# Kernel optimization log

Measured on AMD Instinct MI355X. Metric: run time of the kernel, lower is better.

## Reference

```python
import jax, jax.numpy as jnp
import numpy as np

D_MODEL = 1024
N_HEADS = 16
HEAD_DIM = D_MODEL // N_HEADS


def setup_inputs() -> dict:
    key = jax.random.key(0)
    ks = jax.random.split(key, 5)
    B, T = 4, 4096
    x = jax.random.normal(ks[0], (B, T, D_MODEL), dtype=jnp.float32)
    s = 1.0 / np.sqrt(D_MODEL)
    Wqkv = jax.random.normal(ks[1], (D_MODEL, 3 * D_MODEL), dtype=jnp.float32) * s
    bqkv = jnp.zeros((3 * D_MODEL,), dtype=jnp.float32)
    Wout = jax.random.normal(ks[2], (D_MODEL, D_MODEL), dtype=jnp.float32) * s
    bout = jnp.zeros((D_MODEL,), dtype=jnp.float32)
    return {"x": x, "Wqkv": Wqkv, "bqkv": bqkv, "Wout": Wout, "bout": bout}


def _feature_map(x):
    # elu(x) + 1  (strictly positive feature map)
    return jax.nn.elu(x) + 1.0


def reference(x, Wqkv, bqkv, Wout, bout):
    B, T, C = x.shape
    H, D = N_HEADS, HEAD_DIM
    qkv = x @ Wqkv + bqkv                      # [B,T,3C]
    qkv = qkv.reshape(B, T, 3, H, D)
    qkv = jnp.transpose(qkv, (2, 0, 3, 1, 4))  # [3,B,H,T,D]
    q, k, v = qkv[0], qkv[1], qkv[2]
    scale = D ** 0.25
    q_m = _feature_map(q / scale)
    k_m = _feature_map(k / scale)
    kv = jnp.einsum('bhtd,bhtm->bhdm', k_m, v)     # [B,H,D,D]
    out = jnp.einsum('bhtd,bhdm->bhtm', q_m, kv)   # [B,H,T,D]
    z = q_m.sum(axis=-1, keepdims=True)            # note: sum over feature dim (as in source)
    out = out / (z + 1e-6)
    out = jnp.transpose(out, (0, 2, 1, 3)).reshape(B, T, C)
    return out @ Wout + bout
```

## Files before the change

### kernel.cpp

```cpp
#include <hip/hip_runtime.h>
#include <hip/hip_bf16.h>
#include <math.h>

#define B_ 4
#define T_ 4096
#define H_ 16
#define D_ 64
#define C_ 1024
#define BT_ (B_*T_)

using short8  = __attribute__((ext_vector_type(8))) short;
using floatx4 = __attribute__((ext_vector_type(4))) float;

__device__ __forceinline__ float feature_map(float x) {
    return x > 0.0f ? x + 1.0f : __expf(x);
}
__device__ __forceinline__ unsigned short f2bf(float x) {
    union { __hip_bfloat16 b; unsigned short u; } c;
    c.b = __float2bfloat16(x);
    return c.u;
}
__device__ __forceinline__ float bf2f(unsigned short u) {
    union { unsigned int u; float f; } c;
    c.u = (unsigned)u << 16;
    return c.f;
}
__device__ __forceinline__ void async16(const void* g, void* l) {
    __builtin_amdgcn_global_load_lds(
        (const __attribute__((address_space(1))) void*)g,
        (__attribute__((address_space(3))) void*)l, 16, 0, 0);
}

__global__ __launch_bounds__(256)
void convert_x_kernel(const float4* __restrict__ x, ushort* __restrict__ xb)
{
    const size_t i = (size_t)blockIdx.x * 256 + threadIdx.x;
    const float4 v = x[i];
    *reinterpret_cast<ushort4*>(&xb[i * 4]) =
        make_ushort4(f2bf(v.x), f2bf(v.y), f2bf(v.z), f2bf(v.w));
}

__global__ __launch_bounds__(256)
void transpose_bf16_kernel(const float* __restrict__ W, ushort* __restrict__ WT,
                           int K, int N)
{
    __shared__ float t[32][33];
    const int n0 = blockIdx.x * 32, k0 = blockIdx.y * 32;
    const int r = threadIdx.x >> 5, c = threadIdx.x & 31;
    #pragma unroll
    for (int i = 0; i < 4; i++)
        t[r + 8 * i][c] = W[(size_t)(k0 + r + 8 * i) * N + n0 + c];
    __syncthreads();
    #pragma unroll
    for (int i = 0; i < 4; i++)
        WT[(size_t)(n0 + r + 8 * i) * K + k0 + c] = f2bf(t[c][r + 8 * i]);
}

__global__ __launch_bounds__(256)
void kv_mfma_kernel(const ushort* __restrict__ xb, const ushort* __restrict__ WqkvT,
                    const float* __restrict__ bqkv, float* __restrict__ kv)
{
    __shared__ __align__(16) unsigned char smem[34816];
    ushort* As = (ushort*)smem;
    ushort* Bs = (ushort*)(smem + 8192);
    ushort* kT = (ushort*)smem;
    ushort* vT = kT + 64 * 136;

    const int tid = threadIdx.x;
    const int w = tid >> 6, l = tid & 63;
    const int wm = w >> 1, wn = w & 1;
    const int lr = l & 15, quad = l >> 4;
    const int lk8 = quad * 8;
    const int h = blockIdx.x;
    const int mBase = blockIdx.y * 128;
    const int bb = mBase >> 12;

    const int srow = w * 32 + (l >> 2);
    const int scol = (l & 3) * 8;
    const ushort* gA = xb + (size_t)(mBase + srow) * C_ + scol;
    const int br0 = (srow < 64)      ? (C_ + h * 64 + srow)      : (2 * C_ + h * 64 + srow - 64);
    const int br1 = (srow + 16 < 64) ? (C_ + h * 64 + srow + 16) : (2 * C_ + h * 64 + srow - 48);
    const ushort* gB0 = WqkvT + (size_t)br0 * C_ + scol;
    const ushort* gB1 = WqkvT + (size_t)br1 * C_ + scol;
    void* ldsA = (void*)(smem + w * 2048);
    void* ldsB = (void*)(smem + 8192 + w * 2048);

    floatx4 acc[4][4];
    #pragma unroll
    for (int i = 0; i < 4; i++)
        #pragma unroll
        for (int j = 0; j < 4; j++) acc[i][j] = (floatx4)0.0f;

    for (int k0 = 0; k0 < C_; k0 += 32) {
        __syncthreads();
        async16(gA + k0, ldsA);
        async16(gA + 16 * C_ + k0, (void*)((char*)ldsA + 1024));
        async16(gB0 + k0, ldsB);
        async16(gB1 + k0, (void*)((char*)ldsB + 1024));
        __syncthreads();

        short8 af[4], bf[4];
        #pragma unroll
        for (int mt = 0; mt < 4; mt++)
            af[mt] = *(const short8*)&As[(wm * 64 + mt * 16 + lr) * 32 + lk8];
        #pragma unroll
        for (int nt = 0; nt < 4; nt++)
            bf[nt] = *(const short8*)&Bs[(wn * 64 + nt * 16 + lr) * 32 + lk8];
        #pragma unroll
        for (int mt = 0; mt < 4; mt++)
            #pragma unroll
            for (int nt = 0; nt < 4; nt++)
                acc[mt][nt] = __builtin_amdgcn_mfma_f32_16x16x32_bf16(
                    af[mt], bf[nt], acc[mt][nt], 0, 0, 0);
    }

    const float inv_scale = 0.35355339059327373f;
    const int bbias = (wn ? 2 * C_ : C_) + h * 64;

    __syncthreads();
    {
        ushort* dst = wn ? vT : kT;
        #pragma unroll
        for (int nt = 0; nt < 4; nt++) {
            const int cc = nt * 16 + lr;
            const float bv = bqkv[bbias + cc];
            #pragma unroll
            for (int mt = 0; mt < 4; mt++) {
                float v0 = acc[mt][nt][0] + bv, v1 = acc[mt][nt][1] + bv;
                float v2 = acc[mt][nt][2] + bv, v3 = acc[mt][nt][3] + bv;
                if (wn == 0) {
                    v0 = feature_map(v0 * inv_scale); v1 = feature_map(v1 * inv_scale);
                    v2 = feature_map(v2 * inv_scale); v3 = feature_map(v3 * inv_scale);
                }
                *(ushort4*)&dst[cc * 136 + wm * 64 + mt * 16 + quad * 4] =
                    make_ushort4(f2bf(v0), f2bf(v1), f2bf(v2), f2bf(v3));
            }
        }
    }
    __syncthreads();

    floatx4 acc2[2][2];
    #pragma unroll
    for (int i = 0; i < 2; i++)
        #pragma unroll
        for (int j = 0; j < 2; j++) acc2[i][j] = (floatx4)0.0f;

    #pragma unroll
    for (int kst = 0; kst < 4; kst++) {
        short8 afr[2], bfr[2];
        #pragma unroll
        for (int i = 0; i < 2; i++)
            afr[i] = *(const short8*)&kT[(wm * 32 + i * 16 + lr) * 136 + kst * 32 + lk8];
        #pragma unroll
        for (int j = 0; j < 2; j++)
            bfr[j] = *(const short8*)&vT[(wn * 32 + j * 16 + lr) * 136 + kst * 32 + lk8];
        #pragma unroll
        for (int i = 0; i < 2; i++)
            #pragma unroll
            for (int j = 0; j < 2; j++)
                acc2[i][j] = __builtin_amdgcn_mfma_f32_16x16x32_bf16(
                    afr[i], bfr[j], acc2[i][j], 0, 0, 0);
    }

    float* kvb = kv + (size_t)(bb * H_ + h) * (D_ * D_);
    #pragma unroll
    for (int i = 0; i < 2; i++)
        #pragma unroll
        for (int j = 0; j < 2; j++)
            #pragma unroll
            for (int r = 0; r < 4; r++) {
                const int d = wm * 32 + i * 16 + quad * 4 + r;
                const int m = wn * 32 + j * 16 + lr;
                atomicAdd(&kvb[d * 64 + m], acc2[i][j][r]);
            }
}

__global__ __launch_bounds__(256)
void qattn_mfma_kernel(const ushort* __restrict__ xb, const ushort* __restrict__ WqkvT,
                       const float* __restrict__ bqkv, const float* __restrict__ kv,
                       ushort* __restrict__ attn)
{
    __shared__ __align__(16) unsigned char smem[54272];
    ushort* As  = (ushort*)smem;
    ushort* Bs  = (ushort*)(smem + 8192);
    ushort* qS  = (ushort*)smem;
    ushort* kvT = (ushort*)(smem + 34816);
    float*  zS  = (float*)(smem + 53248);

    const int tid = threadIdx.x;
    const int w = tid >> 6, l = tid & 63;
    const int wm = w >> 1, wn = w & 1;
    const int lr = l & 15, quad = l >> 4;
    const int lk8 = quad * 8;
    const int hp = blockIdx.x;
    const int mBase = blockIdx.y * 128;
    const int bb = mBase >> 12;

    {
        const float* kvg = kv + ((size_t)bb * H_ + hp * 2) * (D_ * D_);
        #pragma unroll
        for (int e = 0; e < 32; e++) {
            const int flat = e * 256 + tid;
            const int hh = flat >> 12, d = (flat >> 6) & 63, m = flat & 63;
            kvT[hh * 4608 + m * 72 + d] = f2bf(kvg[flat]);
        }
    }

    const int srow = w * 32 + (l >> 2);
    const int scol = (l & 3) * 8;
    const ushort* gA = xb + (size_t)(mBase + srow) * C_ + scol;
    const ushort* gB = WqkvT + (size_t)(hp * 128 + srow) * C_ + scol;
    void* ldsA = (void*)(smem + w * 2048);
    void* ldsB = (void*)(smem + 8192 + w * 2048);

    floatx4 acc[4][4];
    #pragma unroll
    for (int i = 0; i < 4; i++)
        #pragma unroll
        for (int j = 0; j < 4; j++) acc[i][j] = (floatx4)0.0f;

    for (int k0 = 0; k0 < C_; k0 += 32) {
        __syncthreads();
        async16(gA + k0, ldsA);
        async16(gA + 16 * C_ + k0, (void*)((char*)ldsA + 1024));
        async16(gB + k0, ldsB);
        async16(gB + 16 * C_ + k0, (void*)((char*)ldsB + 1024));
        __syncthreads();

        short8 af[4], bfr[4];
        #pragma unroll
        for (int mt = 0; mt < 4; mt++)
            af[mt] = *(const short8*)&As[(wm * 64 + mt * 16 + lr) * 32 + lk8];
        #pragma unroll
        for (int nt = 0; nt < 4; nt++)
            bfr[nt] = *(const short8*)&Bs[(wn * 64 + nt * 16 + lr) * 32 + lk8];
        #pragma unroll
        for (int mt = 0; mt < 4; mt++)
            #pragma unroll
            for (int nt = 0; nt < 4; nt++)
                acc[mt][nt] = __builtin_amdgcn_mfma_f32_16x16x32_bf16(
                    af[mt], bfr[nt], acc[mt][nt], 0, 0, 0);
    }

    const float inv_scale = 0.35355339059327373f;

    __syncthreads();
    #pragma unroll
    for (int nt = 0; nt < 4; nt++) {
        const int cc = wn * 64 + nt * 16 + lr;
        const float bv = bqkv[hp * 128 + cc];
        #pragma unroll
        for (int mt = 0; mt < 4; mt++)
            #pragma unroll
            for (int i = 0; i < 4; i++) {
                const int t = wm * 64 + mt * 16 + quad * 4 + i;
                qS[t * 136 + cc] = f2bf(feature_map((acc[mt][nt][i] + bv) * inv_scale));
            }
    }
    __syncthreads();

    {
        const int t = tid & 127, hh = tid >> 7;
        float s = 0.0f;
        #pragma unroll
        for (int c8 = 0; c8 < 8; c8++) {
            const short8 v = *(const short8*)&qS[t * 136 + hh * 64 + c8 * 8];
            #pragma unroll
            for (int j = 0; j < 8; j++) s += bf2f((unsigned short)v[j]);
        }
        zS[hh * 128 + t] = s;
    }

    floatx4 acc3[4][4];
    #pragma unroll
    for (int i = 0; i < 4; i++)
        #pragma unroll
        for (int j = 0; j < 4; j++) acc3[i][j] = (floatx4)0.0f;

    #pragma unroll
    for (int kst = 0; kst < 2; kst++) {
        short8 afr[4], bfr[4];
        #pragma unroll
        for (int mt = 0; mt < 4; mt++)
            afr[mt] = *(const short8*)&qS[(wm * 64 + mt * 16 + lr) * 136 + wn * 64 + kst * 32 + lk8];
        #pragma unroll
        for (int nt = 0; nt < 4; nt++)
            bfr[nt] = *(const short8*)&kvT[wn * 4608 + (nt * 16 + lr) * 72 + kst * 32 + lk8];
        #pragma unroll
        for (int mt = 0; mt < 4; mt++)
            #pragma unroll
            for (int nt = 0; nt < 4; nt++)
                acc3[mt][nt] = __builtin_amdgcn_mfma_f32_16x16x32_bf16(
                    afr[mt], bfr[nt], acc3[mt][nt], 0, 0, 0);
    }
    __syncthreads();

    #pragma unroll
    for (int mt = 0; mt < 4; mt++)
        #pragma unroll
        for (int i = 0; i < 4; i++) {
            const int t = wm * 64 + mt * 16 + quad * 4 + i;
            const float inv = 1.0f / (zS[wn * 128 + t] + 1e-6f);
            #pragma unroll
            for (int nt = 0; nt < 4; nt++)
                qS[t * 136 + wn * 64 + nt * 16 + lr] = f2bf(acc3[mt][nt][i] * inv);
        }
    __syncthreads();

    #pragma unroll
    for (int it = 0; it < 16; it++) {
        const int flat = it * 256 + tid;
        const int row = flat >> 5, c = flat & 31;
        *(ushort4*)&attn[(size_t)(mBase + row) * C_ + hp * 128 + c * 4] =
            *(const ushort4*)&qS[row * 136 + c * 4];
    }
}

__global__ __launch_bounds__(256)
void outproj_mfma_kernel(const ushort* __restrict__ attn, const ushort* __restrict__ WoutT,
                         const float* __restrict__ bout, float* __restrict__ out)
{
    __shared__ __align__(16) unsigned char smem[16384];
    ushort* As = (ushort*)smem;
    ushort* Bs = (ushort*)(smem + 8192);

    const int tid = threadIdx.x;
    const int w = tid >> 6, l = tid & 63;
    const int wm = w >> 1, wn = w & 1;
    const int lr = l & 15, lk8 = (l >> 4) * 8;
    const int mBase = blockIdx.y * 128;
    const int nBase = blockIdx.x * 128;

    const int srow = w * 32 + (l >> 2);
    const int scol = (l & 3) * 8;
    const ushort* gA = attn + (size_t)(mBase + srow) * C_ + scol;
    const ushort* gB = WoutT + (size_t)(nBase + srow) * C_ + scol;
    void* ldsA = (void*)(smem + w * 2048);
    void* ldsB = (void*)(smem + 8192 + w * 2048);

    floatx4 acc[4][4];
    #pragma unroll
    for (int i = 0; i < 4; i++)
        #pragma unroll
        for (int j = 0; j < 4; j++) acc[i][j] = (floatx4)0.0f;

    for (int k0 = 0; k0 < C_; k0 += 32) {
        __syncthreads();
        async16(gA + k0, ldsA);
        async16(gA + 16 * C_ + k0, (void*)((char*)ldsA + 1024));
        async16(gB + k0, ldsB);
        async16(gB + 16 * C_ + k0, (void*)((char*)ldsB + 1024));
        __syncthreads();

        short8 af[4], bfr[4];
        #pragma unroll
        for (int mt = 0; mt < 4; mt++)
            af[mt] = *(const short8*)&As[(wm * 64 + mt * 16 + lr) * 32 + lk8];
        #pragma unroll
        for (int nt = 0; nt < 4; nt++)
            bfr[nt] = *(const short8*)&Bs[(wn * 64 + nt * 16 + lr) * 32 + lk8];
        #pragma unroll
        for (int mt = 0; mt < 4; mt++)
            #pragma unroll
            for (int nt = 0; nt < 4; nt++)
                acc[mt][nt] = __builtin_amdgcn_mfma_f32_16x16x32_bf16(
                    af[mt], bfr[nt], acc[mt][nt], 0, 0, 0);
    }

    #pragma unroll
    for (int mt = 0; mt < 4; mt++)
        #pragma unroll
        for (int nt = 0; nt < 4; nt++) {
            const int cc = nBase + wn * 64 + nt * 16 + lr;
            const float bv = bout[cc];
            #pragma unroll
            for (int i = 0; i < 4; i++) {
                const int rr = mBase + wm * 64 + mt * 16 + (l >> 4) * 4 + i;
                out[(size_t)rr * C_ + cc] = acc[mt][nt][i] + bv;
            }
        }
}

extern "C" void kernel_launch(void* const* d_in, const int* in_sizes, int n_in,
                              void* d_out, int out_size, void* d_ws, size_t ws_size,
                              hipStream_t stream)
{
    const float* x    = (const float*)d_in[0];
    const float* Wqkv = (const float*)d_in[1];
    const float* bqkv = (const float*)d_in[2];
    const float* Wout = (const float*)d_in[3];
    const float* bout = (const float*)d_in[4];
    float* out = (float*)d_out;

    char* ws = (char*)d_ws;
    ushort* xb     = (ushort*)ws;
    ushort* WqkvT  = (ushort*)(ws + 33554432);
    ushort* WoutT  = (ushort*)(ws + 39845888);
    ushort* attn   = (ushort*)(ws + 41943040);
    float*  kv     = (float*) (ws + 75497472);

    hipMemsetAsync(kv, 0, (size_t)B_ * H_ * D_ * D_ * sizeof(float), stream);

    convert_x_kernel<<<(BT_ * C_ / 4) / 256, 256, 0, stream>>>((const float4*)x, xb);
    transpose_bf16_kernel<<<dim3(3 * C_ / 32, C_ / 32), 256, 0, stream>>>(Wqkv, WqkvT, C_, 3 * C_);
    transpose_bf16_kernel<<<dim3(C_ / 32, C_ / 32), 256, 0, stream>>>(Wout, WoutT, C_, C_);

    kv_mfma_kernel<<<dim3(H_, BT_ / 128), 256, 0, stream>>>(xb, WqkvT, bqkv, kv);
    qattn_mfma_kernel<<<dim3(H_ / 2, BT_ / 128), 256, 0, stream>>>(xb, WqkvT, bqkv, kv, attn);
    outproj_mfma_kernel<<<dim3(C_ / 128, BT_ / 128), 256, 0, stream>>>(attn, WoutT, bout, out);
}
```

Measured before the change: 350.1 us.

## Split fused attention into separate QKV GEMM, KV accumulate, and PV kernels

```diff
diff --git a/kernel.cpp b/kernel.cpp
--- a/kernel.cpp
+++ b/kernel.cpp
@@ -57,159 +57,27 @@
 }
 
 __global__ __launch_bounds__(256)
-void kv_mfma_kernel(const ushort* __restrict__ xb, const ushort* __restrict__ WqkvT,
-                    const float* __restrict__ bqkv, float* __restrict__ kv)
-{
-    __shared__ __align__(16) unsigned char smem[34816];
+void qkv_mfma_kernel(const ushort* __restrict__ xb, const ushort* __restrict__ WqkvT,
+                     const float* __restrict__ bqkv,
+                     ushort* __restrict__ qm, ushort* __restrict__ kmT,
+                     ushort* __restrict__ vT)
+{
+    __shared__ __align__(16) unsigned char smem[16384];
     ushort* As = (ushort*)smem;
     ushort* Bs = (ushort*)(smem + 8192);
-    ushort* kT = (ushort*)smem;
-    ushort* vT = kT + 64 * 136;
 
     const int tid = threadIdx.x;
     const int w = tid >> 6, l = tid & 63;
     const int wm = w >> 1, wn = w & 1;
     const int lr = l & 15, quad = l >> 4;
     const int lk8 = quad * 8;
-    const int h = blockIdx.x;
+    const int nBase = blockIdx.x * 128;
     const int mBase = blockIdx.y * 128;
-    const int bb = mBase >> 12;
 
     const int srow = w * 32 + (l >> 2);
     const int scol = (l & 3) * 8;
     const ushort* gA = xb + (size_t)(mBase + srow) * C_ + scol;
-    const int br0 = (srow < 64)      ? (C_ + h * 64 + srow)      : (2 * C_ + h * 64 + srow - 64);
-    const int br1 = (srow + 16 < 64) ? (C_ + h * 64 + srow + 16) : (2 * C_ + h * 64 + srow - 48);
-    const ushort* gB0 = WqkvT + (size_t)br0 * C_ + scol;
-    const ushort* gB1 = WqkvT + (size_t)br1 * C_ + scol;
-    void* ldsA = (void*)(smem + w * 2048);
-    void* ldsB = (void*)(smem + 8192 + w * 2048);
-
-    floatx4 acc[4][4];
-    #pragma unroll
-    for (int i = 0; i < 4; i++)
-        #pragma unroll
-        for (int j = 0; j < 4; j++) acc[i][j] = (floatx4)0.0f;
-
-    for (int k0 = 0; k0 < C_; k0 += 32) {
-        __syncthreads();
-        async16(gA + k0, ldsA);
-        async16(gA + 16 * C_ + k0, (void*)((char*)ldsA + 1024));
-        async16(gB0 + k0, ldsB);
-        async16(gB1 + k0, (void*)((char*)ldsB + 1024));
-        __syncthreads();
-
-        short8 af[4], bf[4];
-        #pragma unroll
-        for (int mt = 0; mt < 4; mt++)
-            af[mt] = *(const short8*)&As[(wm * 64 + mt * 16 + lr) * 32 + lk8];
-        #pragma unroll
-        for (int nt = 0; nt < 4; nt++)
-            bf[nt] = *(const short8*)&Bs[(wn * 64 + nt * 16 + lr) * 32 + lk8];
-        #pragma unroll
-        for (int mt = 0; mt < 4; mt++)
-            #pragma unroll
-            for (int nt = 0; nt < 4; nt++)
-                acc[mt][nt] = __builtin_amdgcn_mfma_f32_16x16x32_bf16(
-                    af[mt], bf[nt], acc[mt][nt], 0, 0, 0);
-    }
-
-    const float inv_scale = 0.35355339059327373f;
-    const int bbias = (wn ? 2 * C_ : C_) + h * 64;
-
-    __syncthreads();
-    {
-        ushort* dst = wn ? vT : kT;
-        #pragma unroll
-        for (int nt = 0; nt < 4; nt++) {
-            const int cc = nt * 16 + lr;
-            const float bv = bqkv[bbias + cc];
-            #pragma unroll
-            for (int mt = 0; mt < 4; mt++) {
-                float v0 = acc[mt][nt][0] + bv, v1 = acc[mt][nt][1] + bv;
-                float v2 = acc[mt][nt][2] + bv, v3 = acc[mt][nt][3] + bv;
-                if (wn == 0) {
-                    v0 = feature_map(v0 * inv_scale); v1 = feature_map(v1 * inv_scale);
-                    v2 = feature_map(v2 * inv_scale); v3 = feature_map(v3 * inv_scale);
-                }
-                *(ushort4*)&dst[cc * 136 + wm * 64 + mt * 16 + quad * 4] =
-                    make_ushort4(f2bf(v0), f2bf(v1), f2bf(v2), f2bf(v3));
-            }
-        }
-    }
-    __syncthreads();
-
-    floatx4 acc2[2][2];
-    #pragma unroll
-    for (int i = 0; i < 2; i++)
-        #pragma unroll
-        for (int j = 0; j < 2; j++) acc2[i][j] = (floatx4)0.0f;
-
-    #pragma unroll
-    for (int kst = 0; kst < 4; kst++) {
-        short8 afr[2], bfr[2];
-        #pragma unroll
-        for (int i = 0; i < 2; i++)
-            afr[i] = *(const short8*)&kT[(wm * 32 + i * 16 + lr) * 136 + kst * 32 + lk8];
-        #pragma unroll
-        for (int j = 0; j < 2; j++)
-            bfr[j] = *(const short8*)&vT[(wn * 32 + j * 16 + lr) * 136 + kst * 32 + lk8];
-        #pragma unroll
-        for (int i = 0; i < 2; i++)
-            #pragma unroll
-            for (int j = 0; j < 2; j++)
-                acc2[i][j] = __builtin_amdgcn_mfma_f32_16x16x32_bf16(
-                    afr[i], bfr[j], acc2[i][j], 0, 0, 0);
-    }
-
-    float* kvb = kv + (size_t)(bb * H_ + h) * (D_ * D_);
-    #pragma unroll
-    for (int i = 0; i < 2; i++)
-        #pragma unroll
-        for (int j = 0; j < 2; j++)
-            #pragma unroll
-            for (int r = 0; r < 4; r++) {
-                const int d = wm * 32 + i * 16 + quad * 4 + r;
-                const int m = wn * 32 + j * 16 + lr;
-                atomicAdd(&kvb[d * 64 + m], acc2[i][j][r]);
-            }
-}
-
-__global__ __launch_bounds__(256)
-void qattn_mfma_kernel(const ushort* __restrict__ xb, const ushort* __restrict__ WqkvT,
-                       const float* __restrict__ bqkv, const float* __restrict__ kv,
-                       ushort* __restrict__ attn)
-{
-    __shared__ __align__(16) unsigned char smem[54272];
-    ushort* As  = (ushort*)smem;
-    ushort* Bs  = (ushort*)(smem + 8192);
-    ushort* qS  = (ushort*)smem;
-    ushort* kvT = (ushort*)(smem + 34816);
-    float*  zS  = (float*)(smem + 53248);
-
-    const int tid = threadIdx.x;
-    const int w = tid >> 6, l = tid & 63;
-    const int wm = w >> 1, wn = w & 1;
-    const int lr = l & 15, quad = l >> 4;
-    const int lk8 = quad * 8;
-    const int hp = blockIdx.x;
-    const int mBase = blockIdx.y * 128;
-    const int bb = mBase >> 12;
-
-    {
-        const float* kvg = kv + ((size_t)bb * H_ + hp * 2) * (D_ * D_);
-        #pragma unroll
-        for (int e = 0; e < 32; e++) {
-            const int flat = e * 256 + tid;
-            const int hh = flat >> 12, d = (flat >> 6) & 63, m = flat & 63;
-            kvT[hh * 4608 + m * 72 + d] = f2bf(kvg[flat]);
-        }
-    }
-
-    const int srow = w * 32 + (l >> 2);
-    const int scol = (l & 3) * 8;
-    const ushort* gA = xb + (size_t)(mBase + srow) * C_ + scol;
-    const ushort* gB = WqkvT + (size_t)(hp * 128 + srow) * C_ + scol;
+    const ushort* gB = WqkvT + (size_t)(nBase + srow) * C_ + scol;
     void* ldsA = (void*)(smem + w * 2048);
     void* ldsB = (void*)(smem + 8192 + w * 2048);
 
@@ -227,92 +95,181 @@
         async16(gB + 16 * C_ + k0, (void*)((char*)ldsB + 1024));
         __syncthreads();
 
-        short8 af[4], bfr[4];
+        short8 af[4], bf[4];
         #pragma unroll
         for (int mt = 0; mt < 4; mt++)
             af[mt] = *(const short8*)&As[(wm * 64 + mt * 16 + lr) * 32 + lk8];
         #pragma unroll
         for (int nt = 0; nt < 4; nt++)
-            bfr[nt] = *(const short8*)&Bs[(wn * 64 + nt * 16 + lr) * 32 + lk8];
+            bf[nt] = *(const short8*)&Bs[(wn * 64 + nt * 16 + lr) * 32 + lk8];
         #pragma unroll
         for (int mt = 0; mt < 4; mt++)
             #pragma unroll
             for (int nt = 0; nt < 4; nt++)
                 acc[mt][nt] = __builtin_amdgcn_mfma_f32_16x16x32_bf16(
-                    af[mt], bfr[nt], acc[mt][nt], 0, 0, 0);
+                    af[mt], bf[nt], acc[mt][nt], 0, 0, 0);
     }
 
     const float inv_scale = 0.35355339059327373f;
-
+    const int seg = nBase >> 10;
+
+    if (seg == 0) {
+        #pragma unroll
+        for (int nt = 0; nt < 4; nt++) {
+            const int c = nBase + wn * 64 + nt * 16 + lr;
+            const float bv = bqkv[c];
+            #pragma unroll
+            for (int mt = 0; mt < 4; mt++)
+                #pragma unroll
+                for (int i = 0; i < 4; i++) {
+                    const int t = mBase + wm * 64 + mt * 16 + quad * 4 + i;
+                    qm[(size_t)t * C_ + c] =
+                        f2bf(feature_map((acc[mt][nt][i] + bv) * inv_scale));
+                }
+        }
+    } else {
+        ushort* dstT = (seg == 1) ? kmT : vT;
+        #pragma unroll
+        for (int nt = 0; nt < 4; nt++) {
+            const int cfull = nBase + wn * 64 + nt * 16 + lr;
+            const int c = cfull - (seg << 10);
+            const float bv = bqkv[cfull];
+            #pragma unroll
+            for (int mt = 0; mt < 4; mt++) {
+                float v0 = acc[mt][nt][0] + bv, v1 = acc[mt][nt][1] + bv;
+                float v2 = acc[mt][nt][2] + bv, v3 = acc[mt][nt][3] + bv;
+                if (seg == 1) {
+                    v0 = feature_map(v0 * inv_scale); v1 = feature_map(v1 * inv_scale);
+                    v2 = feature_map(v2 * inv_scale); v3 = feature_map(v3 * inv_scale);
+                }
+                const int t = mBase + wm * 64 + mt * 16 + quad * 4;
+                *(ushort4*)&dstT[(size_t)c * BT_ + t] =
+                    make_ushort4(f2bf(v0), f2bf(v1), f2bf(v2), f2bf(v3));
+            }
+        }
+    }
+}
+
+__global__ __launch_bounds__(256)
+void kv_accum_kernel(const ushort* __restrict__ kmT, const ushort* __restrict__ vT,
+                     float* __restrict__ kv)
+{
+    const int tid = threadIdx.x;
+    const int w = tid >> 6, l = tid & 63;
+    const int wm = w >> 1, wn = w & 1;
+    const int lr = l & 15, quad = l >> 4;
+    const int bh = blockIdx.y;
+    const int b = bh >> 4, h = bh & 15;
+    const size_t t0 = (size_t)b * T_ + (size_t)blockIdx.x * 512;
+
+    const ushort* Ar = kmT + (size_t)(h * 64 + wm * 32 + lr) * BT_ + t0 + quad * 8;
+    const ushort* Br = vT  + (size_t)(h * 64 + wn * 32 + lr) * BT_ + t0 + quad * 8;
+
+    floatx4 acc[2][2];
+    #pragma unroll
+    for (int i = 0; i < 2; i++)
+        #pragma unroll
+        for (int j = 0; j < 2; j++) acc[i][j] = (floatx4)0.0f;
+
+    #pragma unroll 4
+    for (int tt = 0; tt < 512; tt += 32) {
+        const short8 af0 = *(const short8*)&Ar[tt];
+        const short8 af1 = *(const short8*)&Ar[(size_t)16 * BT_ + tt];
+        const short8 bf0 = *(const short8*)&Br[tt];
+        const short8 bf1 = *(const short8*)&Br[(size_t)16 * BT_ + tt];
+        acc[0][0] = __builtin_amdgcn_mfma_f32_16x16x32_bf16(af0, bf0, acc[0][0], 0, 0, 0);
+        acc[0][1] = __builtin_amdgcn_mfma_f32_16x16x32_bf16(af0, bf1, acc[0][1], 0, 0, 0);
+        acc[1][0] = __builtin_amdgcn_mfma_f32_16x16x32_bf16(af1, bf0, acc[1][0], 0, 0, 0);
+        acc[1][1] = __builtin_amdgcn_mfma_f32_16x16x32_bf16(af1, bf1, acc[1][1], 0, 0, 0);
+    }
+
+    float* kvb = kv + (size_t)bh * (D_ * D_);
+    #pragma unroll
+    for (int i = 0; i < 2; i++)
+        #pragma unroll
+        for (int j = 0; j < 2; j++)
+            #pragma unroll
+            for (int r = 0; r < 4; r++) {
+                const int d = wm * 32 + i * 16 + quad * 4 + r;
+                const int m = wn * 32 + j * 16 + lr;
+                atomicAdd(&kvb[d * 64 + m], acc[i][j][r]);
+            }
+}
+
+__global__ __launch_bounds__(256)
+void pv_kernel(const ushort* __restrict__ qm, const float* __restrict__ kv,
+               ushort* __restrict__ attn)
+{
+    __shared__ ushort kvs[64 * 72];
+    const int tid = threadIdx.x;
+    const int w = tid >> 6, l = tid & 63;
+    const int lr = l & 15, quad = l >> 4;
+    const int h = blockIdx.x;
+    const int tBase = blockIdx.y * 256;
+    const int b = tBase >> 12;
+
+    const float* kvg = kv + ((size_t)b * H_ + h) * (D_ * D_);
+    #pragma unroll
+    for (int e = 0; e < 4; e++) {
+        const int flat = (e * 256 + tid) * 4;
+        const float4 vv = *(const float4*)&kvg[flat];
+        const int d = flat >> 6, m = flat & 63;
+        kvs[(m + 0) * 72 + d] = f2bf(vv.x);
+        kvs[(m + 1) * 72 + d] = f2bf(vv.y);
+        kvs[(m + 2) * 72 + d] = f2bf(vv.z);
+        kvs[(m + 3) * 72 + d] = f2bf(vv.w);
+    }
     __syncthreads();
-    #pragma unroll
-    for (int nt = 0; nt < 4; nt++) {
-        const int cc = wn * 64 + nt * 16 + lr;
-        const float bv = bqkv[hp * 128 + cc];
-        #pragma unroll
-        for (int mt = 0; mt < 4; mt++)
-            #pragma unroll
-            for (int i = 0; i < 4; i++) {
-                const int t = wm * 64 + mt * 16 + quad * 4 + i;
-                qS[t * 136 + cc] = f2bf(feature_map((acc[mt][nt][i] + bv) * inv_scale));
-            }
-    }
-    __syncthreads();
-
-    {
-        const int t = tid & 127, hh = tid >> 7;
-        float s = 0.0f;
-        #pragma unroll
-        for (int c8 = 0; c8 < 8; c8++) {
-            const short8 v = *(const short8*)&qS[t * 136 + hh * 64 + c8 * 8];
-            #pragma unroll
-            for (int j = 0; j < 8; j++) s += bf2f((unsigned short)v[j]);
-        }
-        zS[hh * 128 + t] = s;
-    }
-
-    floatx4 acc3[4][4];
-    #pragma unroll
-    for (int i = 0; i < 4; i++)
-        #pragma unroll
-        for (int j = 0; j < 4; j++) acc3[i][j] = (floatx4)0.0f;
-
-    #pragma unroll
-    for (int kst = 0; kst < 2; kst++) {
-        short8 afr[4], bfr[4];
-        #pragma unroll
-        for (int mt = 0; mt < 4; mt++)
-            afr[mt] = *(const short8*)&qS[(wm * 64 + mt * 16 + lr) * 136 + wn * 64 + kst * 32 + lk8];
-        #pragma unroll
-        for (int nt = 0; nt < 4; nt++)
-            bfr[nt] = *(const short8*)&kvT[wn * 4608 + (nt * 16 + lr) * 72 + kst * 32 + lk8];
-        #pragma unroll
-        for (int mt = 0; mt < 4; mt++)
-            #pragma unroll
-            for (int nt = 0; nt < 4; nt++)
-                acc3[mt][nt] = __builtin_amdgcn_mfma_f32_16x16x32_bf16(
-                    afr[mt], bfr[nt], acc3[mt][nt], 0, 0, 0);
-    }
-    __syncthreads();
-
-    #pragma unroll
-    for (int mt = 0; mt < 4; mt++)
-        #pragma unroll
-        for (int i = 0; i < 4; i++) {
-            const int t = wm * 64 + mt * 16 + quad * 4 + i;
-            const float inv = 1.0f / (zS[wn * 128 + t] + 1e-6f);
-            #pragma unroll
-            for (int nt = 0; nt < 4; nt++)
-                qS[t * 136 + wn * 64 + nt * 16 + lr] = f2bf(acc3[mt][nt][i] * inv);
-        }
-    __syncthreads();
-
-    #pragma unroll
-    for (int it = 0; it < 16; it++) {
-        const int flat = it * 256 + tid;
-        const int row = flat >> 5, c = flat & 31;
-        *(ushort4*)&attn[(size_t)(mBase + row) * C_ + hp * 128 + c * 4] =
-            *(const ushort4*)&qS[row * 136 + c * 4];
+
+    const int tw = tBase + w * 64;
+
+    floatx4 acc[4][4];
+    #pragma unroll
+    for (int i = 0; i < 4; i++)
+        #pragma unroll
+        for (int j = 0; j < 4; j++) acc[i][j] = (floatx4)0.0f;
+
+    float zp[4] = {0.0f, 0.0f, 0.0f, 0.0f};
+
+    #pragma unroll
+    for (int kk = 0; kk < 2; kk++) {
+        short8 bf[4];
+        #pragma unroll
+        for (int tf = 0; tf < 4; tf++) {
+            bf[tf] = *(const short8*)&qm[(size_t)(tw + tf * 16 + lr) * C_
+                                         + h * 64 + kk * 32 + quad * 8];
+            #pragma unroll
+            for (int j = 0; j < 8; j++) zp[tf] += bf2f((unsigned short)bf[tf][j]);
+        }
+        short8 af[4];
+        #pragma unroll
+        for (int mf = 0; mf < 4; mf++)
+            af[mf] = *(const short8*)&kvs[(mf * 16 + lr) * 72 + kk * 32 + quad * 8];
+        #pragma unroll
+        for (int mf = 0; mf < 4; mf++)
+            #pragma unroll
+            for (int tf = 0; tf < 4; tf++)
+                acc[mf][tf] = __builtin_amdgcn_mfma_f32_16x16x32_bf16(
+                    af[mf], bf[tf], acc[mf][tf], 0, 0, 0);
+    }
+
+    #pragma unroll
+    for (int tf = 0; tf < 4; tf++) {
+        zp[tf] += __shfl_xor(zp[tf], 16);
+        zp[tf] += __shfl_xor(zp[tf], 32);
+    }
+
+    #pragma unroll
+    for (int tf = 0; tf < 4; tf++) {
+        const int t = tw + tf * 16 + lr;
+        const float inv = 1.0f / (zp[tf] + 1e-6f);
+        #pragma unroll
+        for (int mf = 0; mf < 4; mf++) {
+            const int m = mf * 16 + quad * 4;
+            *(ushort4*)&attn[(size_t)t * C_ + h * 64 + m] =
+                make_ushort4(f2bf(acc[mf][tf][0] * inv), f2bf(acc[mf][tf][1] * inv),
+                             f2bf(acc[mf][tf][2] * inv), f2bf(acc[mf][tf][3] * inv));
+        }
     }
 }
 
@@ -396,8 +353,11 @@
     ushort* xb     = (ushort*)ws;
     ushort* WqkvT  = (ushort*)(ws + 33554432);
     ushort* WoutT  = (ushort*)(ws + 39845888);
-    ushort* attn   = (ushort*)(ws + 41943040);
+    ushort* vT     = (ushort*)(ws + 41943040);
     float*  kv     = (float*) (ws + 75497472);
+    ushort* attn   = (ushort*)ws;
+    ushort* qm     = (ushort*)d_out;
+    ushort* kmT    = (ushort*)((char*)d_out + 33554432);
 
     hipMemsetAsync(kv, 0, (size_t)B_ * H_ * D_ * D_ * sizeof(float), stream);
 
@@ -405,7 +365,9 @@
     transpose_bf16_kernel<<<dim3(3 * C_ / 32, C_ / 32), 256, 0, stream>>>(Wqkv, WqkvT, C_, 3 * C_);
     transpose_bf16_kernel<<<dim3(C_ / 32, C_ / 32), 256, 0, stream>>>(Wout, WoutT, C_, C_);
 
-    kv_mfma_kernel<<<dim3(H_, BT_ / 128), 256, 0, stream>>>(xb, WqkvT, bqkv, kv);
-    qattn_mfma_kernel<<<dim3(H_ / 2, BT_ / 128), 256, 0, stream>>>(xb, WqkvT, bqkv, kv, attn);
+    qkv_mfma_kernel<<<dim3(3 * C_ / 128, BT_ / 128), 256, 0, stream>>>(
+        xb, WqkvT, bqkv, qm, kmT, vT);
+    kv_accum_kernel<<<dim3(8, B_ * H_), 256, 0, stream>>>(kmT, vT, kv);
+    pv_kernel<<<dim3(H_, BT_ / 256), 256, 0, stream>>>(qm, kv, attn);
     outproj_mfma_kernel<<<dim3(C_ / 128, BT_ / 128), 256, 0, stream>>>(attn, WoutT, bout, out);
 }
```

Result: slower. 374.7 us (+7.0%).
